# Optimization experiments

Measured on AMD Instinct MI355X. Metric: run time of the kernel, lower is better.

The kernel has to match this reference:

```python
import jax, jax.numpy as jnp
import numpy as np
import math

HIDDEN = 256
HEADS = 8
HEAD_DIM = HIDDEN // HEADS
SCALE = math.sqrt(HEAD_DIM)


def setup_inputs() -> dict:
    key = jax.random.key(0)
    ks = jax.random.split(key, 10)
    B, N = 2, 4096
    x = jax.random.normal(ks[0], (B, N, HIDDEN), dtype=jnp.float32)
    pos = jax.random.normal(ks[1], (B, N, 3), dtype=jnp.float32)
    s = 1.0 / math.sqrt(HIDDEN)
    Wq = jax.random.normal(ks[2], (HIDDEN, HIDDEN), dtype=jnp.float32) * s
    bq = jnp.zeros((HIDDEN,), dtype=jnp.float32)
    Wk = jax.random.normal(ks[3], (HIDDEN, HIDDEN), dtype=jnp.float32) * s
    bk = jnp.zeros((HIDDEN,), dtype=jnp.float32)
    Wv = jax.random.normal(ks[4], (HIDDEN, HIDDEN), dtype=jnp.float32) * s
    bv = jnp.zeros((HIDDEN,), dtype=jnp.float32)
    Wo = jax.random.normal(ks[5], (HIDDEN, HIDDEN), dtype=jnp.float32) * s
    bo = jnp.zeros((HIDDEN,), dtype=jnp.float32)
    return {"x": x, "pos": pos, "Wq": Wq, "bq": bq, "Wk": Wk, "bk": bk,
            "Wv": Wv, "bv": bv, "Wo": Wo, "bo": bo}


def _pairwise_dist(pos):
    # Euclidean cdist via the norm trick; clip for numerical safety.
    sq = jnp.sum(pos * pos, axis=-1)  # [B, N]
    d2 = sq[:, :, None] + sq[:, None, :] - 2.0 * jnp.einsum('bic,bjc->bij', pos, pos)
    return jnp.sqrt(jnp.maximum(d2, 0.0))  # [B, N, N]


def reference(x, pos, Wq, bq, Wk, bk, Wv, bv, Wo, bo):
    B, N, _ = x.shape
    # projections -> [B, H, N, Dh]
    def split_heads(t):
        return t.reshape(B, N, HEADS, HEAD_DIM).transpose(0, 2, 1, 3)
    q = split_heads(x @ Wq.T + bq)
    k = split_heads(x @ Wk.T + bk)
    v = split_heads(x @ Wv.T + bv)
    scores = jnp.einsum('bhid,bhjd->bhij', q, k) / SCALE
    dist_bias = -_pairwise_dist(pos) / 10.0  # [B, N, N]
    scores = scores + dist_bias[:, None, :, :]
    attn = jax.nn.softmax(scores, axis=-1)
    out = jnp.einsum('bhij,bhjd->bhid', attn, v)
    out = out.transpose(0, 2, 1, 3).reshape(B, N, HIDDEN)
    return out @ Wo.T + bo
```

## Files before the change

### kernel.cpp

```cpp
#include <hip/hip_runtime.h>

#define BATCH 2
#define SEQ   4096
#define HID   256
#define NHEAD 8
#define DH    32
#define THR_L2 11.5f
#define QSCALE 0.25501639769925074f
#define BIASC (-0.14426950408889634f)

typedef __attribute__((ext_vector_type(8))) _Float16 half8;
typedef __attribute__((ext_vector_type(4))) _Float16 half4;
typedef __attribute__((ext_vector_type(2))) __fp16   fp16x2;
typedef __attribute__((ext_vector_type(4))) float    f32x4;
typedef __attribute__((ext_vector_type(4))) unsigned int uint4v;

__device__ __forceinline__ float fast_exp2(float x) {
    return __builtin_amdgcn_exp2f(x);
}

__global__ void cvt_f32_f16(const float* __restrict__ src,
                            _Float16* __restrict__ dst, int n) {
    int i = (blockIdx.x * blockDim.x + threadIdx.x) * 4;
    if (i >= n) return;
    f32x4 v = *reinterpret_cast<const f32x4*>(src + i);
    half4 h;
#pragma unroll
    for (int c = 0; c < 4; ++c) h[c] = (_Float16)v[c];
    *reinterpret_cast<half4*>(dst + i) = h;
}

__global__ void cvt_w4(const float* __restrict__ a, const float* __restrict__ b,
                       const float* __restrict__ c, const float* __restrict__ d,
                       _Float16* __restrict__ dst) {
    const float* srcs[4] = {a, b, c, d};
    const float* s = srcs[blockIdx.y];
    const int i = (blockIdx.x * blockDim.x + threadIdx.x) * 4;
    f32x4 v = *reinterpret_cast<const f32x4*>(s + i);
    half4 h;
#pragma unroll
    for (int k = 0; k < 4; ++k) h[k] = (_Float16)v[k];
    *reinterpret_cast<half4*>(dst + (size_t)blockIdx.y * HID * HID + i) = h;
}

__global__ __launch_bounds__(256) void qkv_proj(
    const _Float16* __restrict__ xh, const _Float16* __restrict__ Wh,
    const float* __restrict__ bq, const float* __restrict__ bk,
    const float* __restrict__ bv,
    _Float16* __restrict__ Qh, _Float16* __restrict__ Kh,
    _Float16* __restrict__ Vt)
{
    const int z   = blockIdx.z;
    const int m0  = blockIdx.x * 64;
    const int n0  = blockIdx.y * 64;
    const int tid = threadIdx.x;
    const int w   = tid >> 6, lane = tid & 63;
    const int lr  = lane & 15, lg = lane >> 4;
    const int wr  = (w >> 1) * 32, wc = (w & 1) * 32;

    const _Float16* Wp = Wh + (size_t)z * HID * HID;
    const float* bias = (z == 0) ? bq : (z == 1) ? bk : bv;

    f32x4 acc[2][2] = {};
    const int ar = m0 + wr + lr;
    const int br = n0 + wc + lr;
#pragma unroll
    for (int ks = 0; ks < 8; ++ks) {
        const int ko = ks * 32 + lg * 8;
        half8 a0 = *reinterpret_cast<const half8*>(xh + (size_t)ar * HID + ko);
        half8 a1 = *reinterpret_cast<const half8*>(xh + (size_t)(ar + 16) * HID + ko);
        half8 b0 = *reinterpret_cast<const half8*>(Wp + (size_t)br * HID + ko);
        half8 b1 = *reinterpret_cast<const half8*>(Wp + (size_t)(br + 16) * HID + ko);
        acc[0][0] = __builtin_amdgcn_mfma_f32_16x16x32_f16(a0, b0, acc[0][0], 0, 0, 0);
        acc[0][1] = __builtin_amdgcn_mfma_f32_16x16x32_f16(a0, b1, acc[0][1], 0, 0, 0);
        acc[1][0] = __builtin_amdgcn_mfma_f32_16x16x32_f16(a1, b0, acc[1][0], 0, 0, 0);
        acc[1][1] = __builtin_amdgcn_mfma_f32_16x16x32_f16(a1, b1, acc[1][1], 0, 0, 0);
    }
#pragma unroll
    for (int mf = 0; mf < 2; ++mf)
#pragma unroll
    for (int nf = 0; nf < 2; ++nf)
#pragma unroll
    for (int r = 0; r < 4; ++r) {
        const int m  = m0 + wr + mf * 16 + lg * 4 + r;
        const int o  = n0 + wc + nf * 16 + lr;
        const int bb = m >> 12, nn = m & (SEQ - 1);
        const int hh = o >> 5,  dd = o & (DH - 1);
        float v = acc[mf][nf][r] + bias[o];
        if (z == 0) {
            Qh[(((size_t)(bb * NHEAD + hh) * SEQ) + nn) * DH + dd] =
                (_Float16)(v * QSCALE);
        } else if (z == 1) {
            Kh[(((size_t)(bb * NHEAD + hh) * SEQ) + nn) * DH + dd] = (_Float16)v;
        } else {
            const int pp = (nn & ~31) | ((nn & 12) << 1) | ((nn & 16) >> 2) | (nn & 3);
            Vt[(((size_t)(bb * NHEAD + hh) * DH) + dd) * SEQ + pp] = (_Float16)v;
        }
    }
}

__global__ __launch_bounds__(512, 4) void attn_kernel(
    const _Float16* __restrict__ Qh, const _Float16* __restrict__ Kh,
    const _Float16* __restrict__ Vt, const float* __restrict__ pos,
    _Float16* __restrict__ AO)
{
    __shared__ __align__(16) float pi4[16][4];
    __shared__ __align__(16) float pj4[512][4];
    __shared__ __align__(16) float biasL[16][516];
    __shared__ __align__(16) float xposeL[NHEAD][16];

    const int b    = blockIdx.y;
    const int i0   = blockIdx.x * 16;
    const int tid  = threadIdx.x;
    const int w    = tid >> 6;
    const int lane = tid & 63;
    const int lr   = lane & 15, lg = lane >> 4;

    if (tid < 16) {
        const float* p = pos + (size_t)(b * SEQ + i0 + tid) * 3;
        float x = p[0], y = p[1], z = p[2];
        pi4[tid][0] = x; pi4[tid][1] = y; pi4[tid][2] = z;
        pi4[tid][3] = x * x + y * y + z * z;
    }

    const size_t bhh = (size_t)(b * NHEAD + w);
    const _Float16* Qbase = Qh + (bhh * SEQ + i0) * DH;
    const _Float16* Kl  = Kh + bhh * SEQ * DH + (size_t)lr * DH + lg * 8;
    const _Float16* Vl0 = Vt + bhh * DH * SEQ + (size_t)lr * SEQ + lg * 8;
    const _Float16* Vl1 = Vt + bhh * DH * SEQ + (size_t)(16 + lr) * SEQ + lg * 8;

    const half8 aq = *reinterpret_cast<const half8*>(Qbase + (size_t)lr * DH + lg * 8);

    f32x4 acc0 = {}, acc1 = {};
    float mrun = -1e30f, lsum = 0.f;

    float* xw = &xposeL[w][0];
    const float* biasRow = &biasL[lr][0];

    for (int ch = 0; ch < SEQ / 512; ++ch) {
        __syncthreads();
        {
            const float* p = pos + (size_t)(b * SEQ + ch * 512 + tid) * 3;
            float x = p[0], y = p[1], z = p[2];
            pj4[tid][0] = x; pj4[tid][1] = y; pj4[tid][2] = z;
            pj4[tid][3] = x * x + y * y + z * z;
        }
        __syncthreads();
        {
            const int br  = tid & 15;
            const int c0  = (tid >> 4) * 16;
            const float xi = pi4[br][0], yi = pi4[br][1], zi = pi4[br][2], si = pi4[br][3];
#pragma unroll
            for (int k4 = 0; k4 < 4; ++k4) {
                f32x4 o;
#pragma unroll
                for (int k = 0; k < 4; ++k) {
                    const float* pj = &pj4[c0 + k4 * 4 + k][0];
                    float dot = xi * pj[0] + yi * pj[1] + zi * pj[2];
                    float d2  = si + pj[3] - 2.f * dot;
                    o[k] = BIASC * sqrtf(fmaxf(d2, 0.f));
                }
                *reinterpret_cast<f32x4*>(&biasL[br][c0 + k4 * 4]) = o;
            }
        }
        __syncthreads();

        for (int s = 0; s < 8; ++s) {
            const int t  = ch * 8 + s;
            const int jh = t * 64;

            half8 k8[4];
#pragma unroll
            for (int cf = 0; cf < 4; ++cf)
                k8[cf] = *reinterpret_cast<const half8*>(
                    Kl + (size_t)(jh + cf * 16) * DH);
            half8 vc0 = *reinterpret_cast<const half8*>(Vl0 + jh);
            half8 vc1 = *reinterpret_cast<const half8*>(Vl1 + jh);
            half8 vc2 = *reinterpret_cast<const half8*>(Vl0 + jh + 32);
            half8 vc3 = *reinterpret_cast<const half8*>(Vl1 + jh + 32);

            f32x4 vv[4];
            __builtin_amdgcn_s_setprio(1);
#pragma unroll
            for (int cf = 0; cf < 4; ++cf) {
                f32x4 cb = *reinterpret_cast<const f32x4*>(
                    biasRow + s * 64 + cf * 16 + lg * 4);
                vv[cf] = __builtin_amdgcn_mfma_f32_16x16x32_f16(k8[cf], aq, cb, 0, 0, 0);
            }
            __builtin_amdgcn_s_setprio(0);

            float m0 = fmaxf(fmaxf(vv[0][0], vv[0][1]), vv[0][2]);
            float m1 = fmaxf(fmaxf(vv[0][3], vv[1][0]), vv[1][1]);
            float m2 = fmaxf(fmaxf(vv[1][2], vv[1][3]), vv[2][0]);
            float m3 = fmaxf(fmaxf(vv[2][1], vv[2][2]), vv[2][3]);
            float m4 = fmaxf(fmaxf(vv[3][0], vv[3][1]), vv[3][2]);
            float tmax = fmaxf(fmaxf(fmaxf(m0, m1), fmaxf(m2, m3)),
                               fmaxf(m4, vv[3][3]));

            if (!__all(tmax <= mrun + THR_L2)) {
                float tm = tmax;
                tm = fmaxf(tm, __shfl_xor(tm, 16, 64));
                tm = fmaxf(tm, __shfl_xor(tm, 32, 64));
                const float mnew  = fmaxf(mrun, tm);
                const float alpha = fast_exp2(mrun - mnew);
                if (lane < 16) xw[lane] = alpha;
                f32x4 a4 = *reinterpret_cast<const f32x4*>(&xw[lg * 4]);
                lsum *= alpha;
                mrun = mnew;
                acc0 *= a4;
                acc1 *= a4;
            }

            float e00 = fast_exp2(vv[0][0] - mrun), e01 = fast_exp2(vv[0][1] - mrun);
            float e02 = fast_exp2(vv[0][2] - mrun), e03 = fast_exp2(vv[0][3] - mrun);
            float e10 = fast_exp2(vv[1][0] - mrun), e11 = fast_exp2(vv[1][1] - mrun);
            float e12 = fast_exp2(vv[1][2] - mrun), e13 = fast_exp2(vv[1][3] - mrun);
            float e20 = fast_exp2(vv[2][0] - mrun), e21 = fast_exp2(vv[2][1] - mrun);
            float e22 = fast_exp2(vv[2][2] - mrun), e23 = fast_exp2(vv[2][3] - mrun);
            float e30 = fast_exp2(vv[3][0] - mrun), e31 = fast_exp2(vv[3][1] - mrun);
            float e32 = fast_exp2(vv[3][2] - mrun), e33 = fast_exp2(vv[3][3] - mrun);
            lsum += ((e00 + e01) + (e02 + e03)) + ((e10 + e11) + (e12 + e13)) +
                    ((e20 + e21) + (e22 + e23)) + ((e30 + e31) + (e32 + e33));

            uint4v u0, u1;
            u0[0] = __builtin_bit_cast(unsigned int, __builtin_amdgcn_cvt_pkrtz(e00, e01));
            u0[1] = __builtin_bit_cast(unsigned int, __builtin_amdgcn_cvt_pkrtz(e02, e03));
            u0[2] = __builtin_bit_cast(unsigned int, __builtin_amdgcn_cvt_pkrtz(e10, e11));
            u0[3] = __builtin_bit_cast(unsigned int, __builtin_amdgcn_cvt_pkrtz(e12, e13));
            u1[0] = __builtin_bit_cast(unsigned int, __builtin_amdgcn_cvt_pkrtz(e20, e21));
            u1[1] = __builtin_bit_cast(unsigned int, __builtin_amdgcn_cvt_pkrtz(e22, e23));
            u1[2] = __builtin_bit_cast(unsigned int, __builtin_amdgcn_cvt_pkrtz(e30, e31));
            u1[3] = __builtin_bit_cast(unsigned int, __builtin_amdgcn_cvt_pkrtz(e32, e33));
            half8 pa0 = __builtin_bit_cast(half8, u0);
            half8 pa1 = __builtin_bit_cast(half8, u1);

            __builtin_amdgcn_s_setprio(1);
            acc0 = __builtin_amdgcn_mfma_f32_16x16x32_f16(pa0, vc0, acc0, 0, 0, 0);
            acc1 = __builtin_amdgcn_mfma_f32_16x16x32_f16(pa0, vc1, acc1, 0, 0, 0);
            acc0 = __builtin_amdgcn_mfma_f32_16x16x32_f16(pa1, vc2, acc0, 0, 0, 0);
            acc1 = __builtin_amdgcn_mfma_f32_16x16x32_f16(pa1, vc3, acc1, 0, 0, 0);
            __builtin_amdgcn_s_setprio(0);
        }
    }

    lsum += __shfl_xor(lsum, 16, 64);
    lsum += __shfl_xor(lsum, 32, 64);
    const float inv = 1.f / lsum;
    if (lane < 16) xw[lane] = inv;
    f32x4 i4 = *reinterpret_cast<const f32x4*>(&xw[lg * 4]);
#pragma unroll
    for (int t = 0; t < 4; ++t) {
        const size_t row = (size_t)(b * SEQ + i0 + lg * 4 + t) * HID + w * DH;
        AO[row + lr]      = (_Float16)(acc0[t] * i4[t]);
        AO[row + 16 + lr] = (_Float16)(acc1[t] * i4[t]);
    }
}

__global__ __launch_bounds__(256) void out_proj(
    const _Float16* __restrict__ AO, const _Float16* __restrict__ Woh,
    const float* __restrict__ bo, float* __restrict__ out)
{
    const int m0  = blockIdx.x * 64;
    const int n0  = blockIdx.y * 64;
    const int tid = threadIdx.x;
    const int w   = tid >> 6, lane = tid & 63;
    const int lr  = lane & 15, lg = lane >> 4;
    const int wr  = (w >> 1) * 32, wc = (w & 1) * 32;

    f32x4 acc[2][2] = {};
    const int ar = m0 + wr + lr;
    const int br = n0 + wc + lr;
#pragma unroll
    for (int ks = 0; ks < 8; ++ks) {
        const int ko = ks * 32 + lg * 8;
        half8 a0 = *reinterpret_cast<const half8*>(AO + (size_t)ar * HID + ko);
        half8 a1 = *reinterpret_cast<const half8*>(AO + (size_t)(ar + 16) * HID + ko);
        half8 b0 = *reinterpret_cast<const half8*>(Woh + (size_t)br * HID + ko);
        half8 b1 = *reinterpret_cast<const half8*>(Woh + (size_t)(br + 16) * HID + ko);
        acc[0][0] = __builtin_amdgcn_mfma_f32_16x16x32_f16(a0, b0, acc[0][0], 0, 0, 0);
        acc[0][1] = __builtin_amdgcn_mfma_f32_16x16x32_f16(a0, b1, acc[0][1], 0, 0, 0);
        acc[1][0] = __builtin_amdgcn_mfma_f32_16x16x32_f16(a1, b0, acc[1][0], 0, 0, 0);
        acc[1][1] = __builtin_amdgcn_mfma_f32_16x16x32_f16(a1, b1, acc[1][1], 0, 0, 0);
    }
#pragma unroll
    for (int mf = 0; mf < 2; ++mf)
#pragma unroll
    for (int nf = 0; nf < 2; ++nf)
#pragma unroll
    for (int r = 0; r < 4; ++r) {
        const int m = m0 + wr + mf * 16 + lg * 4 + r;
        const int o = n0 + wc + nf * 16 + lr;
        out[(size_t)m * HID + o] = acc[mf][nf][r] + bo[o];
    }
}

extern "C" void kernel_launch(void* const* d_in, const int* in_sizes, int n_in,
                              void* d_out, int out_size, void* d_ws, size_t ws_size,
                              hipStream_t stream)
{
    const float* x   = (const float*)d_in[0];
    const float* pos = (const float*)d_in[1];
    const float* Wq  = (const float*)d_in[2];
    const float* bq  = (const float*)d_in[3];
    const float* Wk  = (const float*)d_in[4];
    const float* bk  = (const float*)d_in[5];
    const float* Wv  = (const float*)d_in[6];
    const float* bv  = (const float*)d_in[7];
    const float* Wo  = (const float*)d_in[8];
    const float* bo  = (const float*)d_in[9];
    float* out = (float*)d_out;

    char* ws = (char*)d_ws;
    _Float16* Qh = (_Float16*)(ws);
    _Float16* Kh = (_Float16*)(ws + (4  << 20));
    _Float16* Vt = (_Float16*)(ws + (8  << 20));
    _Float16* xh = (_Float16*)(ws + (12 << 20));
    _Float16* AO = xh;
    _Float16* Wh = (_Float16*)(ws + (16 << 20));

    const int NX = BATCH * SEQ * HID;
    const int NW = HID * HID;
    cvt_f32_f16<<<NX / 1024, 256, 0, stream>>>(x, xh, NX);
    cvt_w4<<<dim3(NW / 1024, 4), 256, 0, stream>>>(Wq, Wk, Wv, Wo, Wh);

    qkv_proj<<<dim3(BATCH * SEQ / 64, HID / 64, 3), 256, 0, stream>>>(
        xh, Wh, bq, bk, bv, Qh, Kh, Vt);

    attn_kernel<<<dim3(SEQ / 16, BATCH), 512, 0, stream>>>(Qh, Kh, Vt, pos, AO);

    out_proj<<<dim3(BATCH * SEQ / 64, HID / 64), 256, 0, stream>>>(
        AO, Wh + 3 * NW, bo, out);
}
```

Measured before the change: 237.5 us.

## Compute distance bias via MFMA on augmented positions, single-wave blocks with prefetch

Replaces the per-block LDS distance-bias computation with an augmented-position matrix product done on MFMA (pos augmented with -2x, |p|^2, 1), so the squared distance comes from the matrix units and only the sqrt is applied per element. The attention kernel becomes one wave per block (one head per block), removing the __syncthreads and LDS staging, and uses inline-asm global loads with explicit vmcnt waits to double-buffer K tiles and overlap V/Paug loads. The cost is fp16 precision on the squared-distance terms, extra redundant per-head distance computation, and a new preprocessing kernel.

```diff
diff --git a/kernel.cpp b/kernel.cpp
--- a/kernel.cpp
+++ b/kernel.cpp
@@ -41,6 +41,29 @@
 #pragma unroll
     for (int k = 0; k < 4; ++k) h[k] = (_Float16)v[k];
     *reinterpret_cast<half4*>(dst + (size_t)blockIdx.y * HID * HID + i) = h;
+}
+
+__global__ void paug_kernel(const float* __restrict__ pos,
+                            _Float16* __restrict__ Paug) {
+    const int j = blockIdx.x * 256 + threadIdx.x;
+    const float* p = pos + (size_t)j * 3;
+    const float x = p[0], y = p[1], z = p[2];
+    half8 r0;
+#pragma unroll
+    for (int k = 0; k < 8; ++k) r0[k] = (_Float16)0.f;
+    r0[0] = (_Float16)(-2.f * x);
+    r0[1] = (_Float16)(-2.f * y);
+    r0[2] = (_Float16)(-2.f * z);
+    r0[3] = (_Float16)(x * x + y * y + z * z);
+    r0[4] = (_Float16)1.f;
+    half8 zz;
+#pragma unroll
+    for (int k = 0; k < 8; ++k) zz[k] = (_Float16)0.f;
+    _Float16* dst = Paug + (size_t)j * 32;
+    *reinterpret_cast<half8*>(dst)      = r0;
+    *reinterpret_cast<half8*>(dst + 8)  = zz;
+    *reinterpret_cast<half8*>(dst + 16) = zz;
+    *reinterpret_cast<half8*>(dst + 24) = zz;
 }
 
 __global__ __launch_bounds__(256) void qkv_proj(
@@ -99,149 +122,173 @@
     }
 }
 
-__global__ __launch_bounds__(512, 4) void attn_kernel(
+__device__ __forceinline__ void attn_tile(
+    half8 (&kc)[4], half8 (&kn)[4],
+    unsigned long long& ka, unsigned long long& pa,
+    unsigned long long& va0, unsigned long long& va1,
+    half8 aq, half8 qaug, float* xw,
+    float& mrun, float& lsum, f32x4& acc0, f32x4& acc1, int lane, int lg)
+{
+    half8 pg0, pg1, pg2, pg3, vc0, vc1, vc2, vc3;
+    asm volatile(
+        "global_load_dwordx4 %0, %[pa], off\n\t"
+        "global_load_dwordx4 %1, %[pa], off offset:1024\n\t"
+        "global_load_dwordx4 %2, %[pa], off offset:2048\n\t"
+        "global_load_dwordx4 %3, %[pa], off offset:3072\n\t"
+        "global_load_dwordx4 %4, %[va0], off\n\t"
+        "global_load_dwordx4 %5, %[va1], off\n\t"
+        "global_load_dwordx4 %6, %[va0], off offset:64\n\t"
+        "global_load_dwordx4 %7, %[va1], off offset:64\n\t"
+        "global_load_dwordx4 %8, %[ka], off\n\t"
+        "global_load_dwordx4 %9, %[ka], off offset:1024\n\t"
+        "global_load_dwordx4 %10, %[ka], off offset:2048\n\t"
+        "global_load_dwordx4 %11, %[ka], off offset:3072"
+        : "=&v"(pg0), "=&v"(pg1), "=&v"(pg2), "=&v"(pg3),
+          "=&v"(vc0), "=&v"(vc1), "=&v"(vc2), "=&v"(vc3),
+          "=&v"(kn[0]), "=&v"(kn[1]), "=&v"(kn[2]), "=&v"(kn[3])
+        : [pa]"v"(pa), [va0]"v"(va0), [va1]"v"(va1), [ka]"v"(ka));
+    pa += 4096; va0 += 128; va1 += 128; ka += 4096;
+
+    asm volatile("s_waitcnt vmcnt(12)");
+    __builtin_amdgcn_sched_barrier(0);
+    f32x4 z4 = {0.f, 0.f, 0.f, 0.f};
+    f32x4 vv[4];
+    __builtin_amdgcn_s_setprio(1);
+    vv[0] = __builtin_amdgcn_mfma_f32_16x16x32_f16(kc[0], aq, z4, 0, 0, 0);
+    vv[1] = __builtin_amdgcn_mfma_f32_16x16x32_f16(kc[1], aq, z4, 0, 0, 0);
+    vv[2] = __builtin_amdgcn_mfma_f32_16x16x32_f16(kc[2], aq, z4, 0, 0, 0);
+    vv[3] = __builtin_amdgcn_mfma_f32_16x16x32_f16(kc[3], aq, z4, 0, 0, 0);
+    __builtin_amdgcn_s_setprio(0);
+
+    asm volatile("s_waitcnt vmcnt(8)");
+    __builtin_amdgcn_sched_barrier(0);
+    f32x4 dd[4];
+    dd[0] = __builtin_amdgcn_mfma_f32_16x16x32_f16(pg0, qaug, z4, 0, 0, 0);
+    dd[1] = __builtin_amdgcn_mfma_f32_16x16x32_f16(pg1, qaug, z4, 0, 0, 0);
+    dd[2] = __builtin_amdgcn_mfma_f32_16x16x32_f16(pg2, qaug, z4, 0, 0, 0);
+    dd[3] = __builtin_amdgcn_mfma_f32_16x16x32_f16(pg3, qaug, z4, 0, 0, 0);
+#pragma unroll
+    for (int cf = 0; cf < 4; ++cf)
+#pragma unroll
+    for (int t = 0; t < 4; ++t)
+        vv[cf][t] += BIASC * sqrtf(fmaxf(dd[cf][t], 0.f));
+
+    float m0 = fmaxf(fmaxf(vv[0][0], vv[0][1]), vv[0][2]);
+    float m1 = fmaxf(fmaxf(vv[0][3], vv[1][0]), vv[1][1]);
+    float m2 = fmaxf(fmaxf(vv[1][2], vv[1][3]), vv[2][0]);
+    float m3 = fmaxf(fmaxf(vv[2][1], vv[2][2]), vv[2][3]);
+    float m4 = fmaxf(fmaxf(vv[3][0], vv[3][1]), vv[3][2]);
+    float tmax = fmaxf(fmaxf(fmaxf(m0, m1), fmaxf(m2, m3)),
+                       fmaxf(m4, vv[3][3]));
+
+    if (!__all(tmax <= mrun + THR_L2)) {
+        float tm = tmax;
+        tm = fmaxf(tm, __shfl_xor(tm, 16, 64));
+        tm = fmaxf(tm, __shfl_xor(tm, 32, 64));
+        const float mnew  = fmaxf(mrun, tm);
+        const float alpha = fast_exp2(mrun - mnew);
+        if (lane < 16) xw[lane] = alpha;
+        f32x4 a4 = *reinterpret_cast<const f32x4*>(&xw[lg * 4]);
+        lsum *= alpha;
+        mrun = mnew;
+        acc0 *= a4;
+        acc1 *= a4;
+    }
+
+    float e00 = fast_exp2(vv[0][0] - mrun), e01 = fast_exp2(vv[0][1] - mrun);
+    float e02 = fast_exp2(vv[0][2] - mrun), e03 = fast_exp2(vv[0][3] - mrun);
+    float e10 = fast_exp2(vv[1][0] - mrun), e11 = fast_exp2(vv[1][1] - mrun);
+    float e12 = fast_exp2(vv[1][2] - mrun), e13 = fast_exp2(vv[1][3] - mrun);
+    float e20 = fast_exp2(vv[2][0] - mrun), e21 = fast_exp2(vv[2][1] - mrun);
+    float e22 = fast_exp2(vv[2][2] - mrun), e23 = fast_exp2(vv[2][3] - mrun);
+    float e30 = fast_exp2(vv[3][0] - mrun), e31 = fast_exp2(vv[3][1] - mrun);
+    float e32 = fast_exp2(vv[3][2] - mrun), e33 = fast_exp2(vv[3][3] - mrun);
+    lsum += ((e00 + e01) + (e02 + e03)) + ((e10 + e11) + (e12 + e13)) +
+            ((e20 + e21) + (e22 + e23)) + ((e30 + e31) + (e32 + e33));
+
+    uint4v u0, u1;
+    u0[0] = __builtin_bit_cast(unsigned int, __builtin_amdgcn_cvt_pkrtz(e00, e01));
+    u0[1] = __builtin_bit_cast(unsigned int, __builtin_amdgcn_cvt_pkrtz(e02, e03));
+    u0[2] = __builtin_bit_cast(unsigned int, __builtin_amdgcn_cvt_pkrtz(e10, e11));
+    u0[3] = __builtin_bit_cast(unsigned int, __builtin_amdgcn_cvt_pkrtz(e12, e13));
+    u1[0] = __builtin_bit_cast(unsigned int, __builtin_amdgcn_cvt_pkrtz(e20, e21));
+    u1[1] = __builtin_bit_cast(unsigned int, __builtin_amdgcn_cvt_pkrtz(e22, e23));
+    u1[2] = __builtin_bit_cast(unsigned int, __builtin_amdgcn_cvt_pkrtz(e30, e31));
+    u1[3] = __builtin_bit_cast(unsigned int, __builtin_amdgcn_cvt_pkrtz(e32, e33));
+    half8 pa0 = __builtin_bit_cast(half8, u0);
+    half8 pa1 = __builtin_bit_cast(half8, u1);
+
+    asm volatile("s_waitcnt vmcnt(4)");
+    __builtin_amdgcn_sched_barrier(0);
+    __builtin_amdgcn_s_setprio(1);
+    acc0 = __builtin_amdgcn_mfma_f32_16x16x32_f16(pa0, vc0, acc0, 0, 0, 0);
+    acc1 = __builtin_amdgcn_mfma_f32_16x16x32_f16(pa0, vc1, acc1, 0, 0, 0);
+    acc0 = __builtin_amdgcn_mfma_f32_16x16x32_f16(pa1, vc2, acc0, 0, 0, 0);
+    acc1 = __builtin_amdgcn_mfma_f32_16x16x32_f16(pa1, vc3, acc1, 0, 0, 0);
+    __builtin_amdgcn_s_setprio(0);
+}
+
+__global__ __launch_bounds__(64, 4) void attn_kernel(
     const _Float16* __restrict__ Qh, const _Float16* __restrict__ Kh,
-    const _Float16* __restrict__ Vt, const float* __restrict__ pos,
-    _Float16* __restrict__ AO)
-{
-    __shared__ __align__(16) float pi4[16][4];
-    __shared__ __align__(16) float pj4[512][4];
-    __shared__ __align__(16) float biasL[16][516];
-    __shared__ __align__(16) float xposeL[NHEAD][16];
-
-    const int b    = blockIdx.y;
-    const int i0   = blockIdx.x * 16;
-    const int tid  = threadIdx.x;
-    const int w    = tid >> 6;
-    const int lane = tid & 63;
+    const _Float16* __restrict__ Vt, const _Float16* __restrict__ Paug,
+    const float* __restrict__ pos, _Float16* __restrict__ AO)
+{
+    __shared__ float xw[16];
+
+    const int g    = blockIdx.x;
+    const int bh   = g & 15;
+    const int iblk = g >> 4;
+    const int b    = bh >> 3, h = bh & 7;
+    const int i0   = iblk * 16;
+    const int lane = threadIdx.x;
     const int lr   = lane & 15, lg = lane >> 4;
 
-    if (tid < 16) {
-        const float* p = pos + (size_t)(b * SEQ + i0 + tid) * 3;
-        float x = p[0], y = p[1], z = p[2];
-        pi4[tid][0] = x; pi4[tid][1] = y; pi4[tid][2] = z;
-        pi4[tid][3] = x * x + y * y + z * z;
-    }
-
-    const size_t bhh = (size_t)(b * NHEAD + w);
-    const _Float16* Qbase = Qh + (bhh * SEQ + i0) * DH;
-    const _Float16* Kl  = Kh + bhh * SEQ * DH + (size_t)lr * DH + lg * 8;
-    const _Float16* Vl0 = Vt + bhh * DH * SEQ + (size_t)lr * SEQ + lg * 8;
-    const _Float16* Vl1 = Vt + bhh * DH * SEQ + (size_t)(16 + lr) * SEQ + lg * 8;
-
-    const half8 aq = *reinterpret_cast<const half8*>(Qbase + (size_t)lr * DH + lg * 8);
+    const size_t bhh = (size_t)(b * NHEAD + h);
+    const half8 aq = *reinterpret_cast<const half8*>(
+        Qh + (bhh * SEQ + i0 + lr) * DH + lg * 8);
+
+    const float* pp = pos + (size_t)(b * SEQ + i0 + lr) * 3;
+    const float px = pp[0], py = pp[1], pz = pp[2];
+    half8 qaug;
+#pragma unroll
+    for (int k = 0; k < 8; ++k) qaug[k] = (_Float16)0.f;
+    if (lg == 0) {
+        qaug[0] = (_Float16)px;
+        qaug[1] = (_Float16)py;
+        qaug[2] = (_Float16)pz;
+        qaug[3] = (_Float16)1.f;
+        qaug[4] = (_Float16)(px * px + py * py + pz * pz);
+    }
+    asm volatile("" :: "v"(aq), "v"(qaug));
+
+    unsigned long long ka  = (unsigned long long)(Kh + bhh * SEQ * DH +
+                                                  (size_t)lr * DH + lg * 8);
+    unsigned long long pa  = (unsigned long long)(Paug +
+                                 ((size_t)b * SEQ + lr) * 32 + lg * 8);
+    unsigned long long va0 = (unsigned long long)(Vt + bhh * DH * SEQ +
+                                                  (size_t)lr * SEQ + lg * 8);
+    unsigned long long va1 = va0 + (size_t)16 * SEQ * 2;
 
     f32x4 acc0 = {}, acc1 = {};
     float mrun = -1e30f, lsum = 0.f;
 
-    float* xw = &xposeL[w][0];
-    const float* biasRow = &biasL[lr][0];
-
-    for (int ch = 0; ch < SEQ / 512; ++ch) {
-        __syncthreads();
-        {
-            const float* p = pos + (size_t)(b * SEQ + ch * 512 + tid) * 3;
-            float x = p[0], y = p[1], z = p[2];
-            pj4[tid][0] = x; pj4[tid][1] = y; pj4[tid][2] = z;
-            pj4[tid][3] = x * x + y * y + z * z;
-        }
-        __syncthreads();
-        {
-            const int br  = tid & 15;
-            const int c0  = (tid >> 4) * 16;
-            const float xi = pi4[br][0], yi = pi4[br][1], zi = pi4[br][2], si = pi4[br][3];
-#pragma unroll
-            for (int k4 = 0; k4 < 4; ++k4) {
-                f32x4 o;
-#pragma unroll
-                for (int k = 0; k < 4; ++k) {
-                    const float* pj = &pj4[c0 + k4 * 4 + k][0];
-                    float dot = xi * pj[0] + yi * pj[1] + zi * pj[2];
-                    float d2  = si + pj[3] - 2.f * dot;
-                    o[k] = BIASC * sqrtf(fmaxf(d2, 0.f));
-                }
-                *reinterpret_cast<f32x4*>(&biasL[br][c0 + k4 * 4]) = o;
-            }
-        }
-        __syncthreads();
-
-        for (int s = 0; s < 8; ++s) {
-            const int t  = ch * 8 + s;
-            const int jh = t * 64;
-
-            half8 k8[4];
-#pragma unroll
-            for (int cf = 0; cf < 4; ++cf)
-                k8[cf] = *reinterpret_cast<const half8*>(
-                    Kl + (size_t)(jh + cf * 16) * DH);
-            half8 vc0 = *reinterpret_cast<const half8*>(Vl0 + jh);
-            half8 vc1 = *reinterpret_cast<const half8*>(Vl1 + jh);
-            half8 vc2 = *reinterpret_cast<const half8*>(Vl0 + jh + 32);
-            half8 vc3 = *reinterpret_cast<const half8*>(Vl1 + jh + 32);
-
-            f32x4 vv[4];
-            __builtin_amdgcn_s_setprio(1);
-#pragma unroll
-            for (int cf = 0; cf < 4; ++cf) {
-                f32x4 cb = *reinterpret_cast<const f32x4*>(
-                    biasRow + s * 64 + cf * 16 + lg * 4);
-                vv[cf] = __builtin_amdgcn_mfma_f32_16x16x32_f16(k8[cf], aq, cb, 0, 0, 0);
-            }
-            __builtin_amdgcn_s_setprio(0);
-
-            float m0 = fmaxf(fmaxf(vv[0][0], vv[0][1]), vv[0][2]);
-            float m1 = fmaxf(fmaxf(vv[0][3], vv[1][0]), vv[1][1]);
-            float m2 = fmaxf(fmaxf(vv[1][2], vv[1][3]), vv[2][0]);
-            float m3 = fmaxf(fmaxf(vv[2][1], vv[2][2]), vv[2][3]);
-            float m4 = fmaxf(fmaxf(vv[3][0], vv[3][1]), vv[3][2]);
-            float tmax = fmaxf(fmaxf(fmaxf(m0, m1), fmaxf(m2, m3)),
-                               fmaxf(m4, vv[3][3]));
-
-            if (!__all(tmax <= mrun + THR_L2)) {
-                float tm = tmax;
-                tm = fmaxf(tm, __shfl_xor(tm, 16, 64));
-                tm = fmaxf(tm, __shfl_xor(tm, 32, 64));
-                const float mnew  = fmaxf(mrun, tm);
-                const float alpha = fast_exp2(mrun - mnew);
-                if (lane < 16) xw[lane] = alpha;
-                f32x4 a4 = *reinterpret_cast<const f32x4*>(&xw[lg * 4]);
-                lsum *= alpha;
-                mrun = mnew;
-                acc0 *= a4;
-                acc1 *= a4;
-            }
-
-            float e00 = fast_exp2(vv[0][0] - mrun), e01 = fast_exp2(vv[0][1] - mrun);
-            float e02 = fast_exp2(vv[0][2] - mrun), e03 = fast_exp2(vv[0][3] - mrun);
-            float e10 = fast_exp2(vv[1][0] - mrun), e11 = fast_exp2(vv[1][1] - mrun);
-            float e12 = fast_exp2(vv[1][2] - mrun), e13 = fast_exp2(vv[1][3] - mrun);
-            float e20 = fast_exp2(vv[2][0] - mrun), e21 = fast_exp2(vv[2][1] - mrun);
-            float e22 = fast_exp2(vv[2][2] - mrun), e23 = fast_exp2(vv[2][3] - mrun);
-            float e30 = fast_exp2(vv[3][0] - mrun), e31 = fast_exp2(vv[3][1] - mrun);
-            float e32 = fast_exp2(vv[3][2] - mrun), e33 = fast_exp2(vv[3][3] - mrun);
-            lsum += ((e00 + e01) + (e02 + e03)) + ((e10 + e11) + (e12 + e13)) +
-                    ((e20 + e21) + (e22 + e23)) + ((e30 + e31) + (e32 + e33));
-
-            uint4v u0, u1;
-            u0[0] = __builtin_bit_cast(unsigned int, __builtin_amdgcn_cvt_pkrtz(e00, e01));
-            u0[1] = __builtin_bit_cast(unsigned int, __builtin_amdgcn_cvt_pkrtz(e02, e03));
-            u0[2] = __builtin_bit_cast(unsigned int, __builtin_amdgcn_cvt_pkrtz(e10, e11));
-            u0[3] = __builtin_bit_cast(unsigned int, __builtin_amdgcn_cvt_pkrtz(e12, e13));
-            u1[0] = __builtin_bit_cast(unsigned int, __builtin_amdgcn_cvt_pkrtz(e20, e21));
-            u1[1] = __builtin_bit_cast(unsigned int, __builtin_amdgcn_cvt_pkrtz(e22, e23));
-            u1[2] = __builtin_bit_cast(unsigned int, __builtin_amdgcn_cvt_pkrtz(e30, e31));
-            u1[3] = __builtin_bit_cast(unsigned int, __builtin_amdgcn_cvt_pkrtz(e32, e33));
-            half8 pa0 = __builtin_bit_cast(half8, u0);
-            half8 pa1 = __builtin_bit_cast(half8, u1);
-
-            __builtin_amdgcn_s_setprio(1);
-            acc0 = __builtin_amdgcn_mfma_f32_16x16x32_f16(pa0, vc0, acc0, 0, 0, 0);
-            acc1 = __builtin_amdgcn_mfma_f32_16x16x32_f16(pa0, vc1, acc1, 0, 0, 0);
-            acc0 = __builtin_amdgcn_mfma_f32_16x16x32_f16(pa1, vc2, acc0, 0, 0, 0);
-            acc1 = __builtin_amdgcn_mfma_f32_16x16x32_f16(pa1, vc3, acc1, 0, 0, 0);
-            __builtin_amdgcn_s_setprio(0);
-        }
-    }
+    half8 kA[4], kB[4];
+    asm volatile(
+        "global_load_dwordx4 %0, %[ka], off\n\t"
+        "global_load_dwordx4 %1, %[ka], off offset:1024\n\t"
+        "global_load_dwordx4 %2, %[ka], off offset:2048\n\t"
+        "global_load_dwordx4 %3, %[ka], off offset:3072"
+        : "=&v"(kA[0]), "=&v"(kA[1]), "=&v"(kA[2]), "=&v"(kA[3])
+        : [ka]"v"(ka));
+    ka += 4096;
+
+    for (int t = 0; t < SEQ / 64; t += 2) {
+        attn_tile(kA, kB, ka, pa, va0, va1, aq, qaug, xw,
+                  mrun, lsum, acc0, acc1, lane, lg);
+        attn_tile(kB, kA, ka, pa, va0, va1, aq, qaug, xw,
+                  mrun, lsum, acc0, acc1, lane, lg);
+    }
+    asm volatile("s_waitcnt vmcnt(0)");
 
     lsum += __shfl_xor(lsum, 16, 64);
     lsum += __shfl_xor(lsum, 32, 64);
@@ -250,7 +297,7 @@
     f32x4 i4 = *reinterpret_cast<const f32x4*>(&xw[lg * 4]);
 #pragma unroll
     for (int t = 0; t < 4; ++t) {
-        const size_t row = (size_t)(b * SEQ + i0 + lg * 4 + t) * HID + w * DH;
+        const size_t row = (size_t)(b * SEQ + i0 + lg * 4 + t) * HID + h * DH;
         AO[row + lr]      = (_Float16)(acc0[t] * i4[t]);
         AO[row + 16 + lr] = (_Float16)(acc1[t] * i4[t]);
     }
@@ -317,16 +364,19 @@
     _Float16* xh = (_Float16*)(ws + (12 << 20));
     _Float16* AO = xh;
     _Float16* Wh = (_Float16*)(ws + (16 << 20));
+    _Float16* Pg = (_Float16*)(ws + (16 << 20) + (512 << 10));
 
     const int NX = BATCH * SEQ * HID;
     const int NW = HID * HID;
     cvt_f32_f16<<<NX / 1024, 256, 0, stream>>>(x, xh, NX);
     cvt_w4<<<dim3(NW / 1024, 4), 256, 0, stream>>>(Wq, Wk, Wv, Wo, Wh);
+    paug_kernel<<<BATCH * SEQ / 256, 256, 0, stream>>>(pos, Pg);
 
     qkv_proj<<<dim3(BATCH * SEQ / 64, HID / 64, 3), 256, 0, stream>>>(
         xh, Wh, bq, bk, bv, Qh, Kh, Vt);
 
-    attn_kernel<<<dim3(SEQ / 16, BATCH), 512, 0, stream>>>(Qh, Kh, Vt, pos, AO);
+    attn_kernel<<<BATCH * NHEAD * (SEQ / 16), 64, 0, stream>>>(
+        Qh, Kh, Vt, Pg, pos, AO);
 
     out_proj<<<dim3(BATCH * SEQ / 64, HID / 64), 256, 0, stream>>>(
         AO, Wh + 3 * NW, bo, out);
```

After: 292.5 us. 1.23x slower.

## Prefetch K tiles one step ahead with manual waitcnt and remap attention blocks

Applied to the files above, without the earlier changes.

The attention inner loop is split into a helper that issues the V loads for the current tile and the K loads for the next tile as inline-asm global loads. It then waits with explicit vmcnt counts, so K latency overlaps the previous tile's softmax and PV work. Two K register sets alternate across an unrolled pair of tiles. The grid becomes 1D, with the block index remapped so neighbouring blocks interleave the two batches and adjacent query tiles. The cost is hand-managed vmcnt accounting that the compiler cannot check, and one extra prefetch past the end of each head's K data.

```diff
diff --git a/kernel.cpp b/kernel.cpp
--- a/kernel.cpp
+++ b/kernel.cpp
@@ -99,6 +99,94 @@
     }
 }
 
+__device__ __forceinline__ void attn_tile(
+    int s, half8 (&kc)[4], half8 (&kn)[4],
+    unsigned long long& ka, unsigned long long& va0, unsigned long long& va1,
+    half8 aq, const float* __restrict__ biasRow, float* xw,
+    float& mrun, float& lsum, f32x4& acc0, f32x4& acc1, int lane, int lg)
+{
+    half8 vc0, vc1, vc2, vc3;
+    asm volatile(
+        "global_load_dwordx4 %0, %[va0], off\n\t"
+        "global_load_dwordx4 %1, %[va1], off\n\t"
+        "global_load_dwordx4 %2, %[va0], off offset:64\n\t"
+        "global_load_dwordx4 %3, %[va1], off offset:64\n\t"
+        "global_load_dwordx4 %4, %[ka], off\n\t"
+        "global_load_dwordx4 %5, %[ka], off offset:1024\n\t"
+        "global_load_dwordx4 %6, %[ka], off offset:2048\n\t"
+        "global_load_dwordx4 %7, %[ka], off offset:3072"
+        : "=&v"(vc0), "=&v"(vc1), "=&v"(vc2), "=&v"(vc3),
+          "=&v"(kn[0]), "=&v"(kn[1]), "=&v"(kn[2]), "=&v"(kn[3])
+        : [va0]"v"(va0), [va1]"v"(va1), [ka]"v"(ka));
+    va0 += 128; va1 += 128; ka += 4096;
+
+    asm volatile("s_waitcnt vmcnt(8)");
+    __builtin_amdgcn_sched_barrier(0);
+    f32x4 vv[4];
+    __builtin_amdgcn_s_setprio(1);
+#pragma unroll
+    for (int cf = 0; cf < 4; ++cf) {
+        f32x4 cb = *reinterpret_cast<const f32x4*>(
+            biasRow + s * 64 + cf * 16 + lg * 4);
+        vv[cf] = __builtin_amdgcn_mfma_f32_16x16x32_f16(kc[cf], aq, cb, 0, 0, 0);
+    }
+    __builtin_amdgcn_s_setprio(0);
+
+    float m0 = fmaxf(fmaxf(vv[0][0], vv[0][1]), vv[0][2]);
+    float m1 = fmaxf(fmaxf(vv[0][3], vv[1][0]), vv[1][1]);
+    float m2 = fmaxf(fmaxf(vv[1][2], vv[1][3]), vv[2][0]);
+    float m3 = fmaxf(fmaxf(vv[2][1], vv[2][2]), vv[2][3]);
+    float m4 = fmaxf(fmaxf(vv[3][0], vv[3][1]), vv[3][2]);
+    float tmax = fmaxf(fmaxf(fmaxf(m0, m1), fmaxf(m2, m3)),
+                       fmaxf(m4, vv[3][3]));
+
+    if (!__all(tmax <= mrun + THR_L2)) {
+        float tm = tmax;
+        tm = fmaxf(tm, __shfl_xor(tm, 16, 64));
+        tm = fmaxf(tm, __shfl_xor(tm, 32, 64));
+        const float mnew  = fmaxf(mrun, tm);
+        const float alpha = fast_exp2(mrun - mnew);
+        if (lane < 16) xw[lane] = alpha;
+        f32x4 a4 = *reinterpret_cast<const f32x4*>(&xw[lg * 4]);
+        lsum *= alpha;
+        mrun = mnew;
+        acc0 *= a4;
+        acc1 *= a4;
+    }
+
+    float e00 = fast_exp2(vv[0][0] - mrun), e01 = fast_exp2(vv[0][1] - mrun);
+    float e02 = fast_exp2(vv[0][2] - mrun), e03 = fast_exp2(vv[0][3] - mrun);
+    float e10 = fast_exp2(vv[1][0] - mrun), e11 = fast_exp2(vv[1][1] - mrun);
+    float e12 = fast_exp2(vv[1][2] - mrun), e13 = fast_exp2(vv[1][3] - mrun);
+    float e20 = fast_exp2(vv[2][0] - mrun), e21 = fast_exp2(vv[2][1] - mrun);
+    float e22 = fast_exp2(vv[2][2] - mrun), e23 = fast_exp2(vv[2][3] - mrun);
+    float e30 = fast_exp2(vv[3][0] - mrun), e31 = fast_exp2(vv[3][1] - mrun);
+    float e32 = fast_exp2(vv[3][2] - mrun), e33 = fast_exp2(vv[3][3] - mrun);
+    lsum += ((e00 + e01) + (e02 + e03)) + ((e10 + e11) + (e12 + e13)) +
+            ((e20 + e21) + (e22 + e23)) + ((e30 + e31) + (e32 + e33));
+
+    uint4v u0, u1;
+    u0[0] = __builtin_bit_cast(unsigned int, __builtin_amdgcn_cvt_pkrtz(e00, e01));
+    u0[1] = __builtin_bit_cast(unsigned int, __builtin_amdgcn_cvt_pkrtz(e02, e03));
+    u0[2] = __builtin_bit_cast(unsigned int, __builtin_amdgcn_cvt_pkrtz(e10, e11));
+    u0[3] = __builtin_bit_cast(unsigned int, __builtin_amdgcn_cvt_pkrtz(e12, e13));
+    u1[0] = __builtin_bit_cast(unsigned int, __builtin_amdgcn_cvt_pkrtz(e20, e21));
+    u1[1] = __builtin_bit_cast(unsigned int, __builtin_amdgcn_cvt_pkrtz(e22, e23));
+    u1[2] = __builtin_bit_cast(unsigned int, __builtin_amdgcn_cvt_pkrtz(e30, e31));
+    u1[3] = __builtin_bit_cast(unsigned int, __builtin_amdgcn_cvt_pkrtz(e32, e33));
+    half8 pa0 = __builtin_bit_cast(half8, u0);
+    half8 pa1 = __builtin_bit_cast(half8, u1);
+
+    asm volatile("s_waitcnt vmcnt(4)");
+    __builtin_amdgcn_sched_barrier(0);
+    __builtin_amdgcn_s_setprio(1);
+    acc0 = __builtin_amdgcn_mfma_f32_16x16x32_f16(pa0, vc0, acc0, 0, 0, 0);
+    acc1 = __builtin_amdgcn_mfma_f32_16x16x32_f16(pa0, vc1, acc1, 0, 0, 0);
+    acc0 = __builtin_amdgcn_mfma_f32_16x16x32_f16(pa1, vc2, acc0, 0, 0, 0);
+    acc1 = __builtin_amdgcn_mfma_f32_16x16x32_f16(pa1, vc3, acc1, 0, 0, 0);
+    __builtin_amdgcn_s_setprio(0);
+}
+
 __global__ __launch_bounds__(512, 4) void attn_kernel(
     const _Float16* __restrict__ Qh, const _Float16* __restrict__ Kh,
     const _Float16* __restrict__ Vt, const float* __restrict__ pos,
@@ -109,8 +197,10 @@
     __shared__ __align__(16) float biasL[16][516];
     __shared__ __align__(16) float xposeL[NHEAD][16];
 
-    const int b    = blockIdx.y;
-    const int i0   = blockIdx.x * 16;
+    const int g    = blockIdx.x;
+    const int x    = g & 7;
+    const int b    = x >> 2;
+    const int i0   = ((g >> 3) * 4 + (x & 3)) * 16;
     const int tid  = threadIdx.x;
     const int w    = tid >> 6;
     const int lane = tid & 63;
@@ -118,32 +208,44 @@
 
     if (tid < 16) {
         const float* p = pos + (size_t)(b * SEQ + i0 + tid) * 3;
-        float x = p[0], y = p[1], z = p[2];
-        pi4[tid][0] = x; pi4[tid][1] = y; pi4[tid][2] = z;
-        pi4[tid][3] = x * x + y * y + z * z;
+        float xx = p[0], yy = p[1], zz = p[2];
+        pi4[tid][0] = xx; pi4[tid][1] = yy; pi4[tid][2] = zz;
+        pi4[tid][3] = xx * xx + yy * yy + zz * zz;
     }
 
     const size_t bhh = (size_t)(b * NHEAD + w);
-    const _Float16* Qbase = Qh + (bhh * SEQ + i0) * DH;
-    const _Float16* Kl  = Kh + bhh * SEQ * DH + (size_t)lr * DH + lg * 8;
-    const _Float16* Vl0 = Vt + bhh * DH * SEQ + (size_t)lr * SEQ + lg * 8;
-    const _Float16* Vl1 = Vt + bhh * DH * SEQ + (size_t)(16 + lr) * SEQ + lg * 8;
-
-    const half8 aq = *reinterpret_cast<const half8*>(Qbase + (size_t)lr * DH + lg * 8);
+    const half8 aq = *reinterpret_cast<const half8*>(
+        Qh + (bhh * SEQ + i0 + lr) * DH + lg * 8);
+
+    unsigned long long ka  = (unsigned long long)(Kh + bhh * SEQ * DH +
+                                                  (size_t)lr * DH + lg * 8);
+    unsigned long long va0 = (unsigned long long)(Vt + bhh * DH * SEQ +
+                                                  (size_t)lr * SEQ + lg * 8);
+    unsigned long long va1 = va0 + (size_t)16 * SEQ * 2;
 
     f32x4 acc0 = {}, acc1 = {};
     float mrun = -1e30f, lsum = 0.f;
 
     float* xw = &xposeL[w][0];
     const float* biasRow = &biasL[lr][0];
+
+    half8 kA[4], kB[4];
+    asm volatile(
+        "global_load_dwordx4 %0, %[ka], off\n\t"
+        "global_load_dwordx4 %1, %[ka], off offset:1024\n\t"
+        "global_load_dwordx4 %2, %[ka], off offset:2048\n\t"
+        "global_load_dwordx4 %3, %[ka], off offset:3072"
+        : "=&v"(kA[0]), "=&v"(kA[1]), "=&v"(kA[2]), "=&v"(kA[3])
+        : [ka]"v"(ka));
+    ka += 4096;
 
     for (int ch = 0; ch < SEQ / 512; ++ch) {
         __syncthreads();
         {
             const float* p = pos + (size_t)(b * SEQ + ch * 512 + tid) * 3;
-            float x = p[0], y = p[1], z = p[2];
-            pj4[tid][0] = x; pj4[tid][1] = y; pj4[tid][2] = z;
-            pj4[tid][3] = x * x + y * y + z * z;
+            float xx = p[0], yy = p[1], zz = p[2];
+            pj4[tid][0] = xx; pj4[tid][1] = yy; pj4[tid][2] = zz;
+            pj4[tid][3] = xx * xx + yy * yy + zz * zz;
         }
         __syncthreads();
         {
@@ -165,83 +267,14 @@
         }
         __syncthreads();
 
-        for (int s = 0; s < 8; ++s) {
-            const int t  = ch * 8 + s;
-            const int jh = t * 64;
-
-            half8 k8[4];
-#pragma unroll
-            for (int cf = 0; cf < 4; ++cf)
-                k8[cf] = *reinterpret_cast<const half8*>(
-                    Kl + (size_t)(jh + cf * 16) * DH);
-            half8 vc0 = *reinterpret_cast<const half8*>(Vl0 + jh);
-            half8 vc1 = *reinterpret_cast<const half8*>(Vl1 + jh);
-            half8 vc2 = *reinterpret_cast<const half8*>(Vl0 + jh + 32);
-            half8 vc3 = *reinterpret_cast<const half8*>(Vl1 + jh + 32);
-
-            f32x4 vv[4];
-            __builtin_amdgcn_s_setprio(1);
-#pragma unroll
-            for (int cf = 0; cf < 4; ++cf) {
-                f32x4 cb = *reinterpret_cast<const f32x4*>(
-                    biasRow + s * 64 + cf * 16 + lg * 4);
-                vv[cf] = __builtin_amdgcn_mfma_f32_16x16x32_f16(k8[cf], aq, cb, 0, 0, 0);
-            }
-            __builtin_amdgcn_s_setprio(0);
-
-            float m0 = fmaxf(fmaxf(vv[0][0], vv[0][1]), vv[0][2]);
-            float m1 = fmaxf(fmaxf(vv[0][3], vv[1][0]), vv[1][1]);
-            float m2 = fmaxf(fmaxf(vv[1][2], vv[1][3]), vv[2][0]);
-            float m3 = fmaxf(fmaxf(vv[2][1], vv[2][2]), vv[2][3]);
-            float m4 = fmaxf(fmaxf(vv[3][0], vv[3][1]), vv[3][2]);
-            float tmax = fmaxf(fmaxf(fmaxf(m0, m1), fmaxf(m2, m3)),
-                               fmaxf(m4, vv[3][3]));
-
-            if (!__all(tmax <= mrun + THR_L2)) {
-                float tm = tmax;
-                tm = fmaxf(tm, __shfl_xor(tm, 16, 64));
-                tm = fmaxf(tm, __shfl_xor(tm, 32, 64));
-                const float mnew  = fmaxf(mrun, tm);
-                const float alpha = fast_exp2(mrun - mnew);
-                if (lane < 16) xw[lane] = alpha;
-                f32x4 a4 = *reinterpret_cast<const f32x4*>(&xw[lg * 4]);
-                lsum *= alpha;
-                mrun = mnew;
-                acc0 *= a4;
-                acc1 *= a4;
-            }
-
-            float e00 = fast_exp2(vv[0][0] - mrun), e01 = fast_exp2(vv[0][1] - mrun);
-            float e02 = fast_exp2(vv[0][2] - mrun), e03 = fast_exp2(vv[0][3] - mrun);
-            float e10 = fast_exp2(vv[1][0] - mrun), e11 = fast_exp2(vv[1][1] - mrun);
-            float e12 = fast_exp2(vv[1][2] - mrun), e13 = fast_exp2(vv[1][3] - mrun);
-            float e20 = fast_exp2(vv[2][0] - mrun), e21 = fast_exp2(vv[2][1] - mrun);
-            float e22 = fast_exp2(vv[2][2] - mrun), e23 = fast_exp2(vv[2][3] - mrun);
-            float e30 = fast_exp2(vv[3][0] - mrun), e31 = fast_exp2(vv[3][1] - mrun);
-            float e32 = fast_exp2(vv[3][2] - mrun), e33 = fast_exp2(vv[3][3] - mrun);
-            lsum += ((e00 + e01) + (e02 + e03)) + ((e10 + e11) + (e12 + e13)) +
-                    ((e20 + e21) + (e22 + e23)) + ((e30 + e31) + (e32 + e33));
-
-            uint4v u0, u1;
-            u0[0] = __builtin_bit_cast(unsigned int, __builtin_amdgcn_cvt_pkrtz(e00, e01));
-            u0[1] = __builtin_bit_cast(unsigned int, __builtin_amdgcn_cvt_pkrtz(e02, e03));
-            u0[2] = __builtin_bit_cast(unsigned int, __builtin_amdgcn_cvt_pkrtz(e10, e11));
-            u0[3] = __builtin_bit_cast(unsigned int, __builtin_amdgcn_cvt_pkrtz(e12, e13));
-            u1[0] = __builtin_bit_cast(unsigned int, __builtin_amdgcn_cvt_pkrtz(e20, e21));
-            u1[1] = __builtin_bit_cast(unsigned int, __builtin_amdgcn_cvt_pkrtz(e22, e23));
-            u1[2] = __builtin_bit_cast(unsigned int, __builtin_amdgcn_cvt_pkrtz(e30, e31));
-            u1[3] = __builtin_bit_cast(unsigned int, __builtin_amdgcn_cvt_pkrtz(e32, e33));
-            half8 pa0 = __builtin_bit_cast(half8, u0);
-            half8 pa1 = __builtin_bit_cast(half8, u1);
-
-            __builtin_amdgcn_s_setprio(1);
-            acc0 = __builtin_amdgcn_mfma_f32_16x16x32_f16(pa0, vc0, acc0, 0, 0, 0);
-            acc1 = __builtin_amdgcn_mfma_f32_16x16x32_f16(pa0, vc1, acc1, 0, 0, 0);
-            acc0 = __builtin_amdgcn_mfma_f32_16x16x32_f16(pa1, vc2, acc0, 0, 0, 0);
-            acc1 = __builtin_amdgcn_mfma_f32_16x16x32_f16(pa1, vc3, acc1, 0, 0, 0);
-            __builtin_amdgcn_s_setprio(0);
+        for (int s = 0; s < 4; ++s) {
+            attn_tile(2 * s,     kA, kB, ka, va0, va1, aq, biasRow, xw,
+                      mrun, lsum, acc0, acc1, lane, lg);
+            attn_tile(2 * s + 1, kB, kA, ka, va0, va1, aq, biasRow, xw,
+                      mrun, lsum, acc0, acc1, lane, lg);
         }
     }
+    asm volatile("s_waitcnt vmcnt(0)");
 
     lsum += __shfl_xor(lsum, 16, 64);
     lsum += __shfl_xor(lsum, 32, 64);
@@ -326,7 +359,7 @@
     qkv_proj<<<dim3(BATCH * SEQ / 64, HID / 64, 3), 256, 0, stream>>>(
         xh, Wh, bq, bk, bv, Qh, Kh, Vt);
 
-    attn_kernel<<<dim3(SEQ / 16, BATCH), 512, 0, stream>>>(Qh, Kh, Vt, pos, AO);
+    attn_kernel<<<512, 512, 0, stream>>>(Qh, Kh, Vt, pos, AO);
 
     out_proj<<<dim3(BATCH * SEQ / 64, HID / 64), 256, 0, stream>>>(
         AO, Wh + 3 * NW, bo, out);
```

Result: no change. 236.4 us (-0.5%).
